# Kernel optimization log

Measured on AMD Instinct MI355X. Metric: run time of the kernel, lower is better.

Reference implementation:

```python
import jax, jax.numpy as jnp
import numpy as np

N = 50000      # nodes
DEG = 16       # fixed neighbor count per node -> E = N*DEG edges
F_IN = 128
F_OUT = 128


def setup_inputs() -> dict:
    key = jax.random.key(0)
    k = jax.random.split(key, 6)
    E = N * DEG
    x = jax.random.normal(k[0], (N, F_IN), dtype=jnp.float32)
    weight = jax.random.normal(k[1], (F_IN, F_OUT), dtype=jnp.float32) * (1.0 / np.sqrt(F_OUT))
    bias = jax.random.normal(k[2], (F_OUT,), dtype=jnp.float32) * (1.0 / np.sqrt(F_OUT))
    weights_mask = jax.random.normal(k[3], (2 * F_IN, F_IN), dtype=jnp.float32) * (1.0 / np.sqrt(F_IN))
    adj_vals = jax.random.uniform(k[4], (E,), dtype=jnp.float32)
    edge_src = jax.random.randint(k[5], (E,), 0, N, dtype=jnp.int32)   # neighbor ids (add_all flattened)
    edge_dst = jnp.repeat(jnp.arange(N, dtype=jnp.int32), DEG)         # center node ids
    return {"x": x, "weight": weight, "bias": bias, "weights_mask": weights_mask,
            "adj_vals": adj_vals, "edge_src": edge_src, "edge_dst": edge_dst}


def reference(x, weight, bias, weights_mask, adj_vals, edge_src, edge_dst):
    # Per-edge: concat(center, neighbor) -> mask MLP -> sigmoid (dropout omitted: eval mode)
    cen = x[edge_dst]                    # [E, F]
    nei = x[edge_src]                    # [E, F]
    cen_nei = jnp.concatenate([cen, nei], axis=1)          # [E, 2F]
    mask = jax.nn.sigmoid(cen_nei @ weights_mask)          # [E, F]
    # Weighted neighbor sum scattered back to centers, plus self feature
    agg = jax.ops.segment_sum(mask * nei, edge_dst, num_segments=N)   # [N, F]
    x_new = x + agg
    # Dense transform then spmm aggregation (adj given as edge list with values)
    support = x_new @ weight                                # [N, F_out]
    out = jax.ops.segment_sum(adj_vals[:, None] * support[edge_src], edge_dst, num_segments=N)
    return out + bias
```

## Files before the change

kernel.cpp:

```cpp
#include <hip/hip_runtime.h>
#include <stdint.h>
#include <stddef.h>


#define NNODES 50000
#define DEG    16
#define FD     128

#define NEG_LOG2E -1.44269504f

typedef __bf16 bf16x8 __attribute__((ext_vector_type(8)));
typedef short  s16x8  __attribute__((ext_vector_type(8)));
typedef float  f32x4  __attribute__((ext_vector_type(4)));
typedef float  f32x2  __attribute__((ext_vector_type(2)));

__device__ __forceinline__ short f2bf_s(float f) {
    union { float f; uint32_t u; } v; v.f = f;
    uint32_t r = v.u + 0x7fffu + ((v.u >> 16) & 1u);
    return (short)(r >> 16);
}
__device__ __forceinline__ float bflo(uint32_t u) {
    union { uint32_t u; float f; } v; v.u = u << 16;
    return v.f;
}
__device__ __forceinline__ float bfhi(uint32_t u) {
    union { uint32_t u; float f; } v; v.u = u & 0xffff0000u;
    return v.f;
}

__global__ __launch_bounds__(256) void pack_k(const float* __restrict__ wm,
                                              const float* __restrict__ w,
                                              short* __restrict__ wmb,
                                              short* __restrict__ wpack) {
    int tid = blockIdx.x * 256 + threadIdx.x;
    if (tid < 128 * 256) {
        int k = tid >> 8, c = tid & 255;
        float v = (c < 128) ? wm[k * 128 + c] : wm[(128 + k) * 128 + (c - 128)];
        int idx = (((k >> 5) * 16 + (c >> 4)) * 64 + ((k >> 3) & 3) * 16 + (c & 15)) * 8 + (k & 7);
        wmb[idx] = f2bf_s(NEG_LOG2E * v);
    }
    if (tid < 128 * 128) {
        int k = tid >> 7, n = tid & 127;
        int idx = (((k >> 5) * 8 + (n >> 4)) * 64 + ((k >> 3) & 3) * 16 + (n & 15)) * 8 + (k & 7);
        wpack[idx] = f2bf_s(w[tid]);
    }
}

__global__ __launch_bounds__(256) void zy_k(const float* __restrict__ x,
                                            const short* __restrict__ wmb,
                                            short* __restrict__ zbf,
                                            uint32_t* __restrict__ xb,
                                            uint8_t* __restrict__ y8) {
    __shared__ float ct[16 * 260];
    const int tid = threadIdx.x, wave = tid >> 6, lane = tid & 63;
    const int q = lane >> 4, m = lane & 15;
    const int node0 = blockIdx.x * 16;

    f32x4 acc[4];
    #pragma unroll
    for (int nt = 0; nt < 4; ++nt) acc[nt] = (f32x4){0.f, 0.f, 0.f, 0.f};

    #pragma unroll
    for (int kk = 0; kk < 4; ++kk) {
        const float* rp = x + (size_t)(node0 + m) * FD + kk * 32 + q * 8;
        f32x4 lo = *reinterpret_cast<const f32x4*>(rp);
        f32x4 hi = *reinterpret_cast<const f32x4*>(rp + 4);
        bf16x8 a;
        a[0]=(__bf16)lo.x; a[1]=(__bf16)lo.y; a[2]=(__bf16)lo.z; a[3]=(__bf16)lo.w;
        a[4]=(__bf16)hi.x; a[5]=(__bf16)hi.y; a[6]=(__bf16)hi.z; a[7]=(__bf16)hi.w;
        #pragma unroll
        for (int nt = 0; nt < 4; ++nt) {
            int frag = kk * 16 + wave * 4 + nt;
            s16x8 braw = *reinterpret_cast<const s16x8*>(wmb + ((size_t)frag * 64 + lane) * 8);
            acc[nt] = __builtin_amdgcn_mfma_f32_16x16x32_bf16(a, __builtin_bit_cast(bf16x8, braw), acc[nt], 0, 0, 0);
        }
    }
    #pragma unroll
    for (int nt = 0; nt < 4; ++nt)
        #pragma unroll
        for (int i = 0; i < 4; ++i)
            ct[(q * 4 + i) * 260 + wave * 64 + nt * 16 + m] = acc[nt][i];
    __syncthreads();

    const int row = tid >> 4;
    const int c0  = (tid & 15) * 16;
    const int grow = node0 + row;
    if (c0 < 128) {
        uint32_t zo[8];
        #pragma unroll
        for (int j = 0; j < 8; ++j) {
            float v0 = ct[row * 260 + c0 + 2 * j];
            float v1 = ct[row * 260 + c0 + 2 * j + 1];
            zo[j] = (uint32_t)(uint16_t)f2bf_s(v0) | ((uint32_t)(uint16_t)f2bf_s(v1) << 16);
        }
        uint4* dst = reinterpret_cast<uint4*>(zbf + (size_t)grow * FD + c0);
        dst[0] = make_uint4(zo[0], zo[1], zo[2], zo[3]);
        dst[1] = make_uint4(zo[4], zo[5], zo[6], zo[7]);
    } else {
        const int f0 = c0 - 128;
        const float* xr = x + (size_t)grow * FD + f0;
        uint32_t xo[8];
        #pragma unroll
        for (int j = 0; j < 8; ++j) {
            float v0 = xr[2 * j], v1 = xr[2 * j + 1];
            xo[j] = (uint32_t)(uint16_t)f2bf_s(v0) | ((uint32_t)(uint16_t)f2bf_s(v1) << 16);
        }
        uint4* xdst = reinterpret_cast<uint4*>(xb + (size_t)grow * 64 + f0 / 2);
        xdst[0] = make_uint4(xo[0], xo[1], xo[2], xo[3]);
        xdst[1] = make_uint4(xo[4], xo[5], xo[6], xo[7]);
        uint32_t yo[4];
        #pragma unroll
        for (int g = 0; g < 4; ++g) {
            float y0 = __builtin_amdgcn_exp2f(ct[row * 260 + c0 + 4 * g]);
            float y1 = __builtin_amdgcn_exp2f(ct[row * 260 + c0 + 4 * g + 1]);
            float y2 = __builtin_amdgcn_exp2f(ct[row * 260 + c0 + 4 * g + 2]);
            float y3 = __builtin_amdgcn_exp2f(ct[row * 260 + c0 + 4 * g + 3]);
            int u = __builtin_amdgcn_cvt_pk_fp8_f32(y0, y1, 0, false);
            u     = __builtin_amdgcn_cvt_pk_fp8_f32(y2, y3, u, true);
            yo[g] = (uint32_t)u;
        }
        *reinterpret_cast<uint4*>(y8 + (size_t)grow * 128 + f0) = make_uint4(yo[0], yo[1], yo[2], yo[3]);
    }
}

__global__ __launch_bounds__(256) void edge_k(const short* __restrict__ zbf,
                                              const uint32_t* __restrict__ xb,
                                              const uint8_t* __restrict__ y8,
                                              const int* __restrict__ esrc,
                                              uint32_t* __restrict__ xnb) {
    const int tid = threadIdx.x, wave = tid >> 6, lane = tid & 63;
    const int wn0 = blockIdx.x * 16 + wave * 4;

    #pragma unroll 1
    for (int pr = 0; pr < 2; ++pr) {
        const int nuA = __builtin_amdgcn_readfirstlane(wn0 + pr * 2);
        const int nuB = nuA + 1;
        const int* epA = esrc + nuA * DEG;
        const int* epB = esrc + nuB * DEG;
        int sA[16], sB[16];
        #pragma unroll
        for (int e = 0; e < 16; ++e) { sA[e] = epA[e]; sB[e] = epB[e]; }

        uint32_t zA = reinterpret_cast<const uint32_t*>(zbf + (size_t)nuA * FD)[lane];
        uint32_t zB = reinterpret_cast<const uint32_t*>(zbf + (size_t)nuB * FD)[lane];
        uint32_t cAw = xb[(size_t)nuA * 64 + lane];
        uint32_t cBw = xb[(size_t)nuB * 64 + lane];

        uint32_t xA[16], xB[16];
        uint16_t yA[16], yB[16];
        #pragma unroll
        for (int e = 0; e < 16; ++e) {
            xA[e] = xb[(size_t)sA[e] * 64 + lane];
            xB[e] = xb[(size_t)sB[e] * 64 + lane];
            yA[e] = *reinterpret_cast<const uint16_t*>(y8 + (size_t)sA[e] * 128 + 2 * lane);
            yB[e] = *reinterpret_cast<const uint16_t*>(y8 + (size_t)sB[e] * 128 + 2 * lane);
        }

        const float EzA0 = __builtin_amdgcn_exp2f(bflo(zA)), EzA1 = __builtin_amdgcn_exp2f(bfhi(zA));
        const float EzB0 = __builtin_amdgcn_exp2f(bflo(zB)), EzB1 = __builtin_amdgcn_exp2f(bfhi(zB));
        float aA0 = 0.f, aA1 = 0.f, bA0 = 0.f, bA1 = 0.f;
        float aB0 = 0.f, aB1 = 0.f, bB0 = 0.f, bB1 = 0.f;
        #pragma unroll
        for (int e = 0; e < 16; ++e) {
            f32x2 pA = __builtin_amdgcn_cvt_pk_f32_fp8((int)yA[e], false);
            f32x2 pB = __builtin_amdgcn_cvt_pk_f32_fp8((int)yB[e], false);
            float gA0 = __builtin_amdgcn_rcpf(__builtin_fmaf(EzA0, pA.x, 1.f));
            float gA1 = __builtin_amdgcn_rcpf(__builtin_fmaf(EzA1, pA.y, 1.f));
            float gB0 = __builtin_amdgcn_rcpf(__builtin_fmaf(EzB0, pB.x, 1.f));
            float gB1 = __builtin_amdgcn_rcpf(__builtin_fmaf(EzB1, pB.y, 1.f));
            if (e & 1) { bA0 += gA0 * bflo(xA[e]); bA1 += gA1 * bfhi(xA[e]); bB0 += gB0 * bflo(xB[e]); bB1 += gB1 * bfhi(xB[e]); }
            else       { aA0 += gA0 * bflo(xA[e]); aA1 += gA1 * bfhi(xA[e]); aB0 += gB0 * bflo(xB[e]); aB1 += gB1 * bfhi(xB[e]); }
        }
        float xA0 = bflo(cAw) + aA0 + bA0, xA1 = bfhi(cAw) + aA1 + bA1;
        float xB0 = bflo(cBw) + aB0 + bB0, xB1 = bfhi(cBw) + aB1 + bB1;
        xnb[(size_t)nuA * 64 + lane] = (uint32_t)(uint16_t)f2bf_s(xA0) | ((uint32_t)(uint16_t)f2bf_s(xA1) << 16);
        xnb[(size_t)nuB * 64 + lane] = (uint32_t)(uint16_t)f2bf_s(xB0) | ((uint32_t)(uint16_t)f2bf_s(xB1) << 16);
    }
}

__global__ __launch_bounds__(256) void out_k(const uint32_t* __restrict__ xnb,
                                             const float* __restrict__ adj,
                                             const int* __restrict__ esrc,
                                             const short* __restrict__ wpack,
                                             const float* __restrict__ bias,
                                             float* __restrict__ out) {
    __shared__ float xn[16 * 132];
    const int tid = threadIdx.x, wave = tid >> 6, lane = tid & 63;
    const int q = lane >> 4, m = lane & 15;
    const int node0 = blockIdx.x * 16;
    const int wn0 = node0 + wave * 4;

    #pragma unroll 1
    for (int pr = 0; pr < 2; ++pr) {
        const int nuA = __builtin_amdgcn_readfirstlane(wn0 + pr * 2);
        const int nuB = nuA + 1;
        const int* epA = esrc + nuA * DEG;
        const int* epB = esrc + nuB * DEG;
        const float* apA = adj + nuA * DEG;
        const float* apB = adj + nuB * DEG;
        int sA[16], sB[16];
        #pragma unroll
        for (int e = 0; e < 16; ++e) { sA[e] = epA[e]; sB[e] = epB[e]; }
        float wAv[16], wBv[16];
        #pragma unroll
        for (int e = 0; e < 16; ++e) { wAv[e] = apA[e]; wBv[e] = apB[e]; }

        uint32_t uA[16], uB[16];
        #pragma unroll
        for (int e = 0; e < 16; ++e) {
            uA[e] = xnb[(size_t)sA[e] * 64 + lane];
            uB[e] = xnb[(size_t)sB[e] * 64 + lane];
        }

        float aA0 = 0.f, aA1 = 0.f, bA0 = 0.f, bA1 = 0.f;
        float aB0 = 0.f, aB1 = 0.f, bB0 = 0.f, bB1 = 0.f;
        #pragma unroll
        for (int e = 0; e < 16; ++e) {
            float wA = wAv[e], wB = wBv[e];
            if (e & 1) { bA0 += wA * bflo(uA[e]); bA1 += wA * bfhi(uA[e]); bB0 += wB * bflo(uB[e]); bB1 += wB * bfhi(uB[e]); }
            else       { aA0 += wA * bflo(uA[e]); aA1 += wA * bfhi(uA[e]); aB0 += wB * bflo(uB[e]); aB1 += wB * bfhi(uB[e]); }
        }
        const int rA = wave * 4 + pr * 2, rB = rA + 1;
        f32x2 tA; tA.x = aA0 + bA0; tA.y = aA1 + bA1;
        f32x2 tB; tB.x = aB0 + bB0; tB.y = aB1 + bB1;
        *reinterpret_cast<f32x2*>(&xn[rA * 132 + 2 * lane]) = tA;
        *reinterpret_cast<f32x2*>(&xn[rB * 132 + 2 * lane]) = tB;
    }
    __syncthreads();

    f32x4 sacc[2];
    sacc[0] = (f32x4){0.f, 0.f, 0.f, 0.f};
    sacc[1] = (f32x4){0.f, 0.f, 0.f, 0.f};
    #pragma unroll
    for (int kk = 0; kk < 4; ++kk) {
        const float* p = &xn[m * 132 + kk * 32 + q * 8];
        bf16x8 a;
        a[0]=(__bf16)p[0]; a[1]=(__bf16)p[1]; a[2]=(__bf16)p[2]; a[3]=(__bf16)p[3];
        a[4]=(__bf16)p[4]; a[5]=(__bf16)p[5]; a[6]=(__bf16)p[6]; a[7]=(__bf16)p[7];
        #pragma unroll
        for (int t = 0; t < 2; ++t) {
            int nt = wave * 2 + t;
            s16x8 braw = *reinterpret_cast<const s16x8*>(wpack + ((size_t)(kk * 8 + nt) * 64 + lane) * 8);
            sacc[t] = __builtin_amdgcn_mfma_f32_16x16x32_bf16(a, __builtin_bit_cast(bf16x8, braw), sacc[t], 0, 0, 0);
        }
    }
    #pragma unroll
    for (int t = 0; t < 2; ++t) {
        const int f = (wave * 2 + t) * 16 + m;
        const float bv = bias[f];
        #pragma unroll
        for (int i = 0; i < 4; ++i)
            out[(size_t)(node0 + q * 4 + i) * FD + f] = sacc[t][i] + bv;
    }
}

extern "C" void kernel_launch(void* const* d_in, const int* in_sizes, int n_in,
                              void* d_out, int out_size, void* d_ws, size_t ws_size,
                              hipStream_t stream) {
    const float* x      = (const float*)d_in[0];
    const float* weight = (const float*)d_in[1];
    const float* bias   = (const float*)d_in[2];
    const float* wm     = (const float*)d_in[3];
    const float* adj    = (const float*)d_in[4];
    const int*   esrc   = (const int*)d_in[5];

    short*    wmb   = (short*)d_ws;
    short*    wpack = (short*)((char*)d_ws + 65536);
    short*    zbf   = (short*)((char*)d_ws + 98304);
    uint32_t* xnb   = (uint32_t*)((char*)d_ws + 98304 + (size_t)NNODES * FD * 2);
    uint32_t* xb    = (uint32_t*)d_out;
    uint8_t*  y8    = (uint8_t*)d_out + (size_t)NNODES * FD * 2;
    float*    out   = (float*)d_out;

    pack_k <<<128,         256, 0, stream>>>(wm, weight, wmb, wpack);
    zy_k   <<<NNODES / 16, 256, 0, stream>>>(x, wmb, zbf, xb, y8);
    edge_k <<<NNODES / 16, 256, 0, stream>>>(zbf, xb, y8, esrc, xnb);
    out_k  <<<NNODES / 16, 256, 0, stream>>>(xnb, adj, esrc, wpack, bias, out);
}
```

Before: 179.7 us.

## Restructure gather kernels to use 16-byte per-lane loads across edge quarters

The edge and output gather kernels now give each lane 8 features of one edge quarter and issue 16-byte loads per neighbour row, where before each lane made a 4-byte load per edge. Partial sums are then reduced across the four lane groups with xor shuffles, and each group writes one node's row. The exp2 of the center term moves into zy_k, so ezb stores exp2(z) in bf16 instead of z. The goal is fewer, wider memory transactions and more loads in flight, at the cost of extra shuffle reductions and selects, plus bf16 rounding applied after the exponent.

Result: slower. 213.7 us (+19.0%).

```diff
diff --git a/kernel.cpp b/kernel.cpp
--- a/kernel.cpp
+++ b/kernel.cpp
@@ -48,7 +48,7 @@
 
 __global__ __launch_bounds__(256) void zy_k(const float* __restrict__ x,
                                             const short* __restrict__ wmb,
-                                            short* __restrict__ zbf,
+                                            short* __restrict__ ezb,
                                             uint32_t* __restrict__ xb,
                                             uint8_t* __restrict__ y8) {
     __shared__ float ct[16 * 260];
@@ -89,11 +89,11 @@
         uint32_t zo[8];
         #pragma unroll
         for (int j = 0; j < 8; ++j) {
-            float v0 = ct[row * 260 + c0 + 2 * j];
-            float v1 = ct[row * 260 + c0 + 2 * j + 1];
+            float v0 = __builtin_amdgcn_exp2f(ct[row * 260 + c0 + 2 * j]);
+            float v1 = __builtin_amdgcn_exp2f(ct[row * 260 + c0 + 2 * j + 1]);
             zo[j] = (uint32_t)(uint16_t)f2bf_s(v0) | ((uint32_t)(uint16_t)f2bf_s(v1) << 16);
         }
-        uint4* dst = reinterpret_cast<uint4*>(zbf + (size_t)grow * FD + c0);
+        uint4* dst = reinterpret_cast<uint4*>(ezb + (size_t)grow * FD + c0);
         dst[0] = make_uint4(zo[0], zo[1], zo[2], zo[3]);
         dst[1] = make_uint4(zo[4], zo[5], zo[6], zo[7]);
     } else {
@@ -123,59 +123,84 @@
     }
 }
 
-__global__ __launch_bounds__(256) void edge_k(const short* __restrict__ zbf,
+__global__ __launch_bounds__(256) void edge_k(const short* __restrict__ ezb,
                                               const uint32_t* __restrict__ xb,
                                               const uint8_t* __restrict__ y8,
                                               const int* __restrict__ esrc,
                                               uint32_t* __restrict__ xnb) {
     const int tid = threadIdx.x, wave = tid >> 6, lane = tid & 63;
-    const int wn0 = blockIdx.x * 16 + wave * 4;
-
-    #pragma unroll 1
-    for (int pr = 0; pr < 2; ++pr) {
-        const int nuA = __builtin_amdgcn_readfirstlane(wn0 + pr * 2);
-        const int nuB = nuA + 1;
-        const int* epA = esrc + nuA * DEG;
-        const int* epB = esrc + nuB * DEG;
-        int sA[16], sB[16];
-        #pragma unroll
-        for (int e = 0; e < 16; ++e) { sA[e] = epA[e]; sB[e] = epB[e]; }
-
-        uint32_t zA = reinterpret_cast<const uint32_t*>(zbf + (size_t)nuA * FD)[lane];
-        uint32_t zB = reinterpret_cast<const uint32_t*>(zbf + (size_t)nuB * FD)[lane];
-        uint32_t cAw = xb[(size_t)nuA * 64 + lane];
-        uint32_t cBw = xb[(size_t)nuB * 64 + lane];
-
-        uint32_t xA[16], xB[16];
-        uint16_t yA[16], yB[16];
-        #pragma unroll
-        for (int e = 0; e < 16; ++e) {
-            xA[e] = xb[(size_t)sA[e] * 64 + lane];
-            xB[e] = xb[(size_t)sB[e] * 64 + lane];
-            yA[e] = *reinterpret_cast<const uint16_t*>(y8 + (size_t)sA[e] * 128 + 2 * lane);
-            yB[e] = *reinterpret_cast<const uint16_t*>(y8 + (size_t)sB[e] * 128 + 2 * lane);
-        }
-
-        const float EzA0 = __builtin_amdgcn_exp2f(bflo(zA)), EzA1 = __builtin_amdgcn_exp2f(bfhi(zA));
-        const float EzB0 = __builtin_amdgcn_exp2f(bflo(zB)), EzB1 = __builtin_amdgcn_exp2f(bfhi(zB));
-        float aA0 = 0.f, aA1 = 0.f, bA0 = 0.f, bA1 = 0.f;
-        float aB0 = 0.f, aB1 = 0.f, bB0 = 0.f, bB1 = 0.f;
-        #pragma unroll
-        for (int e = 0; e < 16; ++e) {
-            f32x2 pA = __builtin_amdgcn_cvt_pk_f32_fp8((int)yA[e], false);
-            f32x2 pB = __builtin_amdgcn_cvt_pk_f32_fp8((int)yB[e], false);
-            float gA0 = __builtin_amdgcn_rcpf(__builtin_fmaf(EzA0, pA.x, 1.f));
-            float gA1 = __builtin_amdgcn_rcpf(__builtin_fmaf(EzA1, pA.y, 1.f));
-            float gB0 = __builtin_amdgcn_rcpf(__builtin_fmaf(EzB0, pB.x, 1.f));
-            float gB1 = __builtin_amdgcn_rcpf(__builtin_fmaf(EzB1, pB.y, 1.f));
-            if (e & 1) { bA0 += gA0 * bflo(xA[e]); bA1 += gA1 * bfhi(xA[e]); bB0 += gB0 * bflo(xB[e]); bB1 += gB1 * bfhi(xB[e]); }
-            else       { aA0 += gA0 * bflo(xA[e]); aA1 += gA1 * bfhi(xA[e]); aB0 += gB0 * bflo(xB[e]); aB1 += gB1 * bfhi(xB[e]); }
-        }
-        float xA0 = bflo(cAw) + aA0 + bA0, xA1 = bfhi(cAw) + aA1 + bA1;
-        float xB0 = bflo(cBw) + aB0 + bB0, xB1 = bfhi(cBw) + aB1 + bB1;
-        xnb[(size_t)nuA * 64 + lane] = (uint32_t)(uint16_t)f2bf_s(xA0) | ((uint32_t)(uint16_t)f2bf_s(xA1) << 16);
-        xnb[(size_t)nuB * 64 + lane] = (uint32_t)(uint16_t)f2bf_s(xB0) | ((uint32_t)(uint16_t)f2bf_s(xB1) << 16);
-    }
+    const int q = lane >> 4, li = lane & 15;
+    const int n0 = __builtin_amdgcn_readfirstlane(blockIdx.x * 16 + wave * 4);
+
+    float acc[4][8];
+    #pragma unroll
+    for (int d = 0; d < 4; ++d)
+        #pragma unroll
+        for (int j = 0; j < 8; ++j) acc[d][j] = 0.f;
+
+    #pragma unroll
+    for (int d = 0; d < 4; ++d) {
+        const int nd = n0 + d;
+        const int* ep = esrc + nd * DEG;
+        int se[4];
+        #pragma unroll
+        for (int i = 0; i < 4; ++i) se[i] = ep[i * 4 + q];
+
+        uint4 xw[4]; uint2 yw[4];
+        #pragma unroll
+        for (int i = 0; i < 4; ++i) {
+            xw[i] = *reinterpret_cast<const uint4*>(xb + (size_t)se[i] * 64 + li * 4);
+            yw[i] = *reinterpret_cast<const uint2*>(y8 + (size_t)se[i] * 128 + li * 8);
+        }
+        uint4 ez = *reinterpret_cast<const uint4*>(
+            reinterpret_cast<const uint32_t*>(ezb) + (size_t)nd * 64 + li * 4);
+        float Ez[8] = {bflo(ez.x), bfhi(ez.x), bflo(ez.y), bfhi(ez.y),
+                       bflo(ez.z), bfhi(ez.z), bflo(ez.w), bfhi(ez.w)};
+        #pragma unroll
+        for (int i = 0; i < 4; ++i) {
+            f32x2 p0 = __builtin_amdgcn_cvt_pk_f32_fp8((int)yw[i].x, false);
+            f32x2 p1 = __builtin_amdgcn_cvt_pk_f32_fp8((int)yw[i].x, true);
+            f32x2 p2 = __builtin_amdgcn_cvt_pk_f32_fp8((int)yw[i].y, false);
+            f32x2 p3 = __builtin_amdgcn_cvt_pk_f32_fp8((int)yw[i].y, true);
+            float E[8]  = {p0.x, p0.y, p1.x, p1.y, p2.x, p2.y, p3.x, p3.y};
+            float xf[8] = {bflo(xw[i].x), bfhi(xw[i].x), bflo(xw[i].y), bfhi(xw[i].y),
+                           bflo(xw[i].z), bfhi(xw[i].z), bflo(xw[i].w), bfhi(xw[i].w)};
+            #pragma unroll
+            for (int j = 0; j < 8; ++j) {
+                float g = __builtin_amdgcn_rcpf(__builtin_fmaf(Ez[j], E[j], 1.f));
+                acc[d][j] = __builtin_fmaf(g, xf[j], acc[d][j]);
+            }
+        }
+    }
+
+    #pragma unroll
+    for (int d = 0; d < 4; ++d)
+        #pragma unroll
+        for (int j = 0; j < 8; ++j) {
+            float v = acc[d][j];
+            v += __shfl_xor(v, 16, 64);
+            v += __shfl_xor(v, 32, 64);
+            acc[d][j] = v;
+        }
+
+    const bool q1 = (q & 1) != 0, q2 = (q & 2) != 0;
+    uint4 cw = *reinterpret_cast<const uint4*>(xb + (size_t)(n0 + q) * 64 + li * 4);
+    uint32_t cwv[4] = {cw.x, cw.y, cw.z, cw.w};
+    uint32_t outw[4];
+    #pragma unroll
+    for (int k = 0; k < 4; ++k) {
+        float t0 = q1 ? acc[1][2 * k]     : acc[0][2 * k];
+        float t1 = q1 ? acc[3][2 * k]     : acc[2][2 * k];
+        float slo = q2 ? t1 : t0;
+        float u0 = q1 ? acc[1][2 * k + 1] : acc[0][2 * k + 1];
+        float u1 = q1 ? acc[3][2 * k + 1] : acc[2][2 * k + 1];
+        float shi = q2 ? u1 : u0;
+        float r0 = bflo(cwv[k]) + slo;
+        float r1 = bfhi(cwv[k]) + shi;
+        outw[k] = (uint32_t)(uint16_t)f2bf_s(r0) | ((uint32_t)(uint16_t)f2bf_s(r1) << 16);
+    }
+    *reinterpret_cast<uint4*>(xnb + (size_t)(n0 + q) * 64 + li * 4) =
+        make_uint4(outw[0], outw[1], outw[2], outw[3]);
 }
 
 __global__ __launch_bounds__(256) void out_k(const uint32_t* __restrict__ xnb,
@@ -187,45 +212,61 @@
     __shared__ float xn[16 * 132];
     const int tid = threadIdx.x, wave = tid >> 6, lane = tid & 63;
     const int q = lane >> 4, m = lane & 15;
+    const int li = m;
     const int node0 = blockIdx.x * 16;
-    const int wn0 = node0 + wave * 4;
-
-    #pragma unroll 1
-    for (int pr = 0; pr < 2; ++pr) {
-        const int nuA = __builtin_amdgcn_readfirstlane(wn0 + pr * 2);
-        const int nuB = nuA + 1;
-        const int* epA = esrc + nuA * DEG;
-        const int* epB = esrc + nuB * DEG;
-        const float* apA = adj + nuA * DEG;
-        const float* apB = adj + nuB * DEG;
-        int sA[16], sB[16];
-        #pragma unroll
-        for (int e = 0; e < 16; ++e) { sA[e] = epA[e]; sB[e] = epB[e]; }
-        float wAv[16], wBv[16];
-        #pragma unroll
-        for (int e = 0; e < 16; ++e) { wAv[e] = apA[e]; wBv[e] = apB[e]; }
-
-        uint32_t uA[16], uB[16];
-        #pragma unroll
-        for (int e = 0; e < 16; ++e) {
-            uA[e] = xnb[(size_t)sA[e] * 64 + lane];
-            uB[e] = xnb[(size_t)sB[e] * 64 + lane];
-        }
-
-        float aA0 = 0.f, aA1 = 0.f, bA0 = 0.f, bA1 = 0.f;
-        float aB0 = 0.f, aB1 = 0.f, bB0 = 0.f, bB1 = 0.f;
-        #pragma unroll
-        for (int e = 0; e < 16; ++e) {
-            float wA = wAv[e], wB = wBv[e];
-            if (e & 1) { bA0 += wA * bflo(uA[e]); bA1 += wA * bfhi(uA[e]); bB0 += wB * bflo(uB[e]); bB1 += wB * bfhi(uB[e]); }
-            else       { aA0 += wA * bflo(uA[e]); aA1 += wA * bfhi(uA[e]); aB0 += wB * bflo(uB[e]); aB1 += wB * bfhi(uB[e]); }
-        }
-        const int rA = wave * 4 + pr * 2, rB = rA + 1;
-        f32x2 tA; tA.x = aA0 + bA0; tA.y = aA1 + bA1;
-        f32x2 tB; tB.x = aB0 + bB0; tB.y = aB1 + bB1;
-        *reinterpret_cast<f32x2*>(&xn[rA * 132 + 2 * lane]) = tA;
-        *reinterpret_cast<f32x2*>(&xn[rB * 132 + 2 * lane]) = tB;
-    }
+    const int n0 = __builtin_amdgcn_readfirstlane(node0 + wave * 4);
+
+    float acc[4][8];
+    #pragma unroll
+    for (int d = 0; d < 4; ++d)
+        #pragma unroll
+        for (int j = 0; j < 8; ++j) acc[d][j] = 0.f;
+
+    #pragma unroll
+    for (int d = 0; d < 4; ++d) {
+        const int nd = n0 + d;
+        const int* ep = esrc + nd * DEG;
+        const float* ap = adj + nd * DEG;
+        int se[4]; float wv[4];
+        #pragma unroll
+        for (int i = 0; i < 4; ++i) { se[i] = ep[i * 4 + q]; wv[i] = ap[i * 4 + q]; }
+
+        uint4 uw[4];
+        #pragma unroll
+        for (int i = 0; i < 4; ++i)
+            uw[i] = *reinterpret_cast<const uint4*>(xnb + (size_t)se[i] * 64 + li * 4);
+
+        #pragma unroll
+        for (int i = 0; i < 4; ++i) {
+            float xf[8] = {bflo(uw[i].x), bfhi(uw[i].x), bflo(uw[i].y), bfhi(uw[i].y),
+                           bflo(uw[i].z), bfhi(uw[i].z), bflo(uw[i].w), bfhi(uw[i].w)};
+            #pragma unroll
+            for (int j = 0; j < 8; ++j)
+                acc[d][j] = __builtin_fmaf(wv[i], xf[j], acc[d][j]);
+        }
+    }
+
+    #pragma unroll
+    for (int d = 0; d < 4; ++d)
+        #pragma unroll
+        for (int j = 0; j < 8; ++j) {
+            float v = acc[d][j];
+            v += __shfl_xor(v, 16, 64);
+            v += __shfl_xor(v, 32, 64);
+            acc[d][j] = v;
+        }
+
+    const bool q1 = (q & 1) != 0, q2 = (q & 2) != 0;
+    const int r = wave * 4 + q;
+    float fin[8];
+    #pragma unroll
+    for (int j = 0; j < 8; ++j) {
+        float t0 = q1 ? acc[1][j] : acc[0][j];
+        float t1 = q1 ? acc[3][j] : acc[2][j];
+        fin[j] = q2 ? t1 : t0;
+    }
+    *reinterpret_cast<f32x4*>(&xn[r * 132 + li * 8])     = (f32x4){fin[0], fin[1], fin[2], fin[3]};
+    *reinterpret_cast<f32x4*>(&xn[r * 132 + li * 8 + 4]) = (f32x4){fin[4], fin[5], fin[6], fin[7]};
     __syncthreads();
 
     f32x4 sacc[2];
@@ -266,14 +307,14 @@
 
     short*    wmb   = (short*)d_ws;
     short*    wpack = (short*)((char*)d_ws + 65536);
-    short*    zbf   = (short*)((char*)d_ws + 98304);
+    short*    ezb   = (short*)((char*)d_ws + 98304);
     uint32_t* xnb   = (uint32_t*)((char*)d_ws + 98304 + (size_t)NNODES * FD * 2);
     uint32_t* xb    = (uint32_t*)d_out;
     uint8_t*  y8    = (uint8_t*)d_out + (size_t)NNODES * FD * 2;
     float*    out   = (float*)d_out;
 
     pack_k <<<128,         256, 0, stream>>>(wm, weight, wmb, wpack);
-    zy_k   <<<NNODES / 16, 256, 0, stream>>>(x, wmb, zbf, xb, y8);
-    edge_k <<<NNODES / 16, 256, 0, stream>>>(zbf, xb, y8, esrc, xnb);
+    zy_k   <<<NNODES / 16, 256, 0, stream>>>(x, wmb, ezb, xb, y8);
+    edge_k <<<NNODES / 16, 256, 0, stream>>>(ezb, xb, y8, esrc, xnb);
     out_k  <<<NNODES / 16, 256, 0, stream>>>(xnb, adj, esrc, wpack, bias, out);
 }
```
